# Kernel optimization log

Hardware: AMD Instinct MI355X
Metric: run time of the kernel (lower is better)

Reference implementation:

```python
import jax, jax.numpy as jnp
import numpy as np

B, T, D, H1, H2, O = 256, 200, 1250, 100, 20, 2
P = 0.2  # dropout prob (training=True in the original forward)


def setup_inputs() -> dict:
    key = jax.random.key(0)
    ks = jax.random.split(key, 13)
    s1 = 1.0 / np.sqrt(H1)  # torch nn.RNN init: U(-1/sqrt(hidden), 1/sqrt(hidden))
    s2 = 1.0 / np.sqrt(H2)
    sf = 1.0 / np.sqrt(H2)  # fc fan_in = 20
    u = lambda k, shape, s: jax.random.uniform(k, shape, jnp.float32, -s, s)
    keep = 1.0 - P
    return {
        "x": jax.random.normal(ks[0], (B, T, D), jnp.float32),
        "W_ih1": u(ks[1], (H1, D), s1),
        "W_hh1": u(ks[2], (H1, H1), s1),
        "b_ih1": u(ks[3], (H1,), s1),
        "b_hh1": u(ks[4], (H1,), s1),
        "W_ih2": u(ks[5], (H2, H1), s2),
        "W_hh2": u(ks[6], (H2, H2), s2),
        "b_ih2": u(ks[7], (H2,), s2),
        "b_hh2": u(ks[8], (H2,), s2),
        "W_fc": u(ks[9], (O, H2), sf),
        "b_fc": u(ks[10], (O,), sf),
        # pre-sampled inverted-dropout masks (training=True), scaled by 1/keep
        "mask1": jax.random.bernoulli(ks[11], keep, (B, T, H1)).astype(jnp.float32) / keep,
        "mask2": jax.random.bernoulli(ks[12], keep, (B, T, H2)).astype(jnp.float32) / keep,
    }


def _relu_rnn(x, W_ih, W_hh, b_ih, b_hh):
    # x: [B,T,Din] -> outputs [B,T,H]. Hoist the input projection out of the scan.
    pre = jnp.einsum("btd,hd->bth", x, W_ih) + b_ih + b_hh  # [B,T,H]
    h0 = jnp.zeros((x.shape[0], W_hh.shape[0]), x.dtype)

    def step(h, pre_t):
        h = jax.nn.relu(pre_t + h @ W_hh.T)
        return h, h

    _, out = jax.lax.scan(step, h0, jnp.swapaxes(pre, 0, 1))  # [T,B,H]
    return jnp.swapaxes(out, 0, 1)


def reference(x, W_ih1, W_hh1, b_ih1, b_hh1, W_ih2, W_hh2, b_ih2, b_hh2,
              W_fc, b_fc, mask1, mask2):
    out = _relu_rnn(x, W_ih1, W_hh1, b_ih1, b_hh1) * mask1          # rnn1 + dropout
    out = _relu_rnn(out, W_ih2, W_hh2, b_ih2, b_hh2) * mask2        # rnn2 + dropout
    return out[:, -1, :] @ W_fc.T + b_fc                            # fc on last step
```

## Files before the change

kernel.cpp:

```cpp
#include <hip/hip_runtime.h>

#define NB 256
#define TT 200
#define DD 1250
#define H1 100
#define H2 20
#define NO 2

#define BM 64
#define GRID_A (51200 / BM)
#define KC 64
#define NCH 20
#define WR 112
#define KPAD 1280

typedef __attribute__((ext_vector_type(4))) float f32x4;
typedef __attribute__((ext_vector_type(8))) short s16x8;

__device__ __forceinline__ unsigned short f2bf(float f) {
    unsigned u = __builtin_bit_cast(unsigned, f);
    u += 0x7FFFu + ((u >> 16) & 1u);
    return (unsigned short)(u >> 16);
}
__device__ __forceinline__ float bf2f(unsigned short s) {
    unsigned u = ((unsigned)s) << 16;
    return __builtin_bit_cast(float, u);
}

#define GLL(srcp, dstp) __builtin_amdgcn_global_load_lds( \
    (const __attribute__((address_space(1))) void*)(srcp), \
    (__attribute__((address_space(3))) void*)(dstp), 16, 0, 0)

#define STEP_BARRIER() do {                                             \
    asm volatile("s_waitcnt lgkmcnt(0)\n\ts_barrier" ::: "memory");     \
    __builtin_amdgcn_sched_barrier(0);                                  \
} while (0)

__global__ void prep_w(const float* __restrict__ Wih1, unsigned short* __restrict__ w_ws)
{
    const int idx = blockIdx.x * 256 + threadIdx.x;
    if (idx >= WR * KPAD / 4) return;
    const int r  = idx / (KPAD / 4);
    const int k4 = (idx - r * (KPAD / 4)) * 4;
    unsigned short o[4];
    #pragma unroll
    for (int e = 0; e < 4; ++e) {
        const int k = k4 + e;
        o[e] = (r < H1 && k < DD) ? f2bf(Wih1[r * DD + k]) : (unsigned short)0;
    }
    uint2 pk;
    pk.x = (unsigned)o[0] | ((unsigned)o[1] << 16);
    pk.y = (unsigned)o[2] | ((unsigned)o[3] << 16);
    *(uint2*)&w_ws[r * KPAD + k4] = pk;
}

__launch_bounds__(256, 4)
__global__ void gemm_pre(const float* __restrict__ x,
                         const unsigned short* __restrict__ w_ws,
                         unsigned short* __restrict__ preT)
{
    __shared__ __align__(16) float          a_sf[2][BM * 64];
    __shared__ __align__(16) unsigned short w_sh[2][WR * 64];

    const int tid = threadIdx.x;
    const int bid = blockIdx.x;
    const int wv  = tid >> 6;
    const int ln  = tid & 63;
    const int c16 = ln & 15;
    const int kgrp = ln >> 4;

    f32x4 acc[7];
    #pragma unroll
    for (int i = 0; i < 7; ++i)
        #pragma unroll
        for (int c = 0; c < 4; ++c) acc[i][c] = 0.f;

    auto agll = [&](int k0, int buf) {
        #pragma unroll
        for (int q = 0; q < 4; ++q) {
            const int idx  = tid + q * 256;
            const int row  = idx >> 4;
            const int segp = idx & 15;
            const int segl = segp ^ (row & 15);
            const float* src = x + (size_t)(bid * BM + row) * DD + k0 + segl * 4;
            GLL(src, &a_sf[buf][idx * 4]);
        }
    };
    auto wgll = [&](int k0, int buf) {
        #pragma unroll
        for (int q = 0; q < 4; ++q) {
            const int idx = tid + q * 256;
            if (idx < WR * 8) {
                const int row = idx >> 3;
                const int c8p = idx & 7;
                const int c8l = c8p ^ (row & 7);
                const unsigned short* src = w_ws + row * KPAD + k0 + c8l * 8;
                GLL(src, &w_sh[buf][idx * 8]);
            }
        }
    };

    auto mfma_chunk = [&](int buf) {
        #pragma unroll
        for (int s = 0; s < 2; ++s) {
            const int row_a = wv * 16 + c16;
            const int sb = s * 8 + kgrp * 2;
            const int sp0 = (sb + 0) ^ (row_a & 15);
            const int sp1 = (sb + 1) ^ (row_a & 15);
            const float4 av0 = *(const float4*)&a_sf[buf][row_a * 64 + sp0 * 4];
            const float4 av1 = *(const float4*)&a_sf[buf][row_a * 64 + sp1 * 4];
            const s16x8 af = {
                (short)f2bf(av0.x), (short)f2bf(av0.y),
                (short)f2bf(av0.z), (short)f2bf(av0.w),
                (short)f2bf(av1.x), (short)f2bf(av1.y),
                (short)f2bf(av1.z), (short)f2bf(av1.w) };
            #pragma unroll
            for (int nt = 0; nt < 7; ++nt) {
                const int row_b = nt * 16 + c16;
                const int c8  = s * 4 + kgrp;
                const int c8p = c8 ^ (row_b & 7);
                const s16x8 bf = *(const s16x8*)&w_sh[buf][row_b * 64 + c8p * 8];
                acc[nt] = __builtin_amdgcn_mfma_f32_16x16x32_bf16(af, bf, acc[nt], 0, 0, 0);
            }
        }
    };

    float4 ta[4];
    #pragma unroll
    for (int q = 0; q < 4; ++q) {
        const int idx  = tid + q * 256;
        const int row  = idx >> 4;
        const int segl = idx & 15;
        const int gk   = 19 * KC + segl * 4;
        const float* xp = x + (size_t)(bid * BM + row) * DD + gk;
        float4 v;
        v.x = (gk + 0 < DD) ? xp[0] : 0.f;
        v.y = (gk + 1 < DD) ? xp[1] : 0.f;
        v.z = (gk + 2 < DD) ? xp[2] : 0.f;
        v.w = (gk + 3 < DD) ? xp[3] : 0.f;
        ta[q] = v;
    }

    agll(0, 0);
    wgll(0, 0);

    for (int kc = 0; kc < 19; ++kc) {
        const int buf = kc & 1;
        __syncthreads();
        if (kc + 1 < 19) agll((kc + 1) * KC, buf ^ 1);
        wgll((kc + 1) * KC, buf ^ 1);
        mfma_chunk(buf);
    }

    #pragma unroll
    for (int q = 0; q < 4; ++q) {
        const int idx  = tid + q * 256;
        const int row  = idx >> 4;
        const int segl = idx & 15;
        const int sp   = segl ^ (row & 15);
        *(float4*)&a_sf[1][row * 64 + sp * 4] = ta[q];
    }
    __syncthreads();
    mfma_chunk(1);

    const int rg = bid * BM + wv * 16 + (kgrp << 2);
    #pragma unroll
    for (int nt = 0; nt < 7; ++nt) {
        const int col = nt * 16 + c16;
        if (col < H1) {
            #pragma unroll
            for (int r = 0; r < 4; ++r)
                preT[(size_t)(rg + r) * H1 + col] = f2bf(acc[nt][r]);
        }
    }
}

#define FMA4(W, PTR) { const float4 hv_ = *(const float4*)(PTR);            \
    a0 = fmaf((W).x, hv_.x, a0); a1 = fmaf((W).y, hv_.y, a1);               \
    a2 = fmaf((W).z, hv_.z, a2); a3 = fmaf((W).w, hv_.w, a3); }

#define CH 8
#define NCHK 25

__launch_bounds__(320, 1)
__global__ void scan_rnn(const unsigned short* __restrict__ preT,
                         const float* __restrict__ Whh1,
                         const float* __restrict__ bih1,
                         const float* __restrict__ bhh1,
                         const float* __restrict__ Wih2,
                         const float* __restrict__ Whh2,
                         const float* __restrict__ bih2,
                         const float* __restrict__ bhh2,
                         const float* __restrict__ Wfc,
                         const float* __restrict__ bfc,
                         const float* __restrict__ mask1,
                         const float* __restrict__ mask2,
                         float* __restrict__ out)
{
    __shared__ alignas(16) float h1_s[2][104];
    __shared__ alignas(16) float c_s[2][120];
    __shared__ alignas(16) float h2f_s[H2];
    __shared__ alignas(16) float m_lds[2][CH * H1];
    __shared__ alignas(16) float p_lds[2][CH * H1];

    const int tid = threadIdx.x;
    const int b   = blockIdx.x;
    const float* m1b = mask1 + (size_t)b * TT * H1;
    const unsigned short* pTb = preT + (size_t)b * TT * H1;

    const int h = tid >> 1;
    const int p = tid & 1;
    const bool l1t = (tid < 200);
    const bool l2t = (tid >= 256 && tid < 256 + 2 * H2);
    const int k2 = (tid - 256) >> 1;
    const int p3 = (tid - 256) & 1;

    float4 w00{}, w01{}, w02{}, w03{}, w04{}, w05{}, w06{}, w07{},
           w08{}, w09{}, w10{}, w11{}, w12{}, w13{}, w14{};
    float b1 = 0.f, b2 = 0.f;

    if (l1t) {
        const float* wr = Whh1 + h * H1 + p * 52;
        w00 = *(const float4*)(wr +  0); w01 = *(const float4*)(wr +  4);
        w02 = *(const float4*)(wr +  8); w03 = *(const float4*)(wr + 12);
        w04 = *(const float4*)(wr + 16); w05 = *(const float4*)(wr + 20);
        w06 = *(const float4*)(wr + 24); w07 = *(const float4*)(wr + 28);
        w08 = *(const float4*)(wr + 32); w09 = *(const float4*)(wr + 36);
        w10 = *(const float4*)(wr + 40); w11 = *(const float4*)(wr + 44);
        if (p == 0) { w12 = *(const float4*)(wr + 48); b1 = bih1[h] + bhh1[h]; }
    } else if (l2t) {
        if (p3 == 0) {
            const float* wr = Wih2 + k2 * H1;
            w00 = *(const float4*)(wr +  0); w01 = *(const float4*)(wr +  4);
            w02 = *(const float4*)(wr +  8); w03 = *(const float4*)(wr + 12);
            w04 = *(const float4*)(wr + 16); w05 = *(const float4*)(wr + 20);
            w06 = *(const float4*)(wr + 24); w07 = *(const float4*)(wr + 28);
            w08 = *(const float4*)(wr + 32); w09 = *(const float4*)(wr + 36);
            w10 = *(const float4*)(wr + 40); w11 = *(const float4*)(wr + 44);
            w12 = *(const float4*)(wr + 48); w13 = *(const float4*)(wr + 52);
            w14 = *(const float4*)(wr + 56);
            b2 = bih2[k2] + bhh2[k2];
        } else {
            const float* wr = Wih2 + k2 * H1 + 60;
            w00 = *(const float4*)(wr +  0); w01 = *(const float4*)(wr +  4);
            w02 = *(const float4*)(wr +  8); w03 = *(const float4*)(wr + 12);
            w04 = *(const float4*)(wr + 16); w05 = *(const float4*)(wr + 20);
            w06 = *(const float4*)(wr + 24); w07 = *(const float4*)(wr + 28);
            w08 = *(const float4*)(wr + 32); w09 = *(const float4*)(wr + 36);
            const float* wh = Whh2 + k2 * H2;
            w10 = *(const float4*)(wh +  0); w11 = *(const float4*)(wh +  4);
            w12 = *(const float4*)(wh +  8); w13 = *(const float4*)(wh + 12);
            w14 = *(const float4*)(wh + 16);
        }
    }

    for (int i = tid; i < 104; i += 320) { h1_s[0][i] = 0.f; h1_s[1][i] = 0.f; }
    for (int i = tid; i < 120; i += 320) { c_s[0][i] = 0.f; c_s[1][i] = 0.f; }

    if (tid < 200) {
        const float4 mv = *(const float4*)&m1b[tid * 4];
        *(float4*)&m_lds[0][tid * 4] = mv;
    } else if (tid < 300) {
        const s16x8 pv = *(const s16x8*)&pTb[(tid - 200) * 8];
        float* dst = &p_lds[0][(tid - 200) * 8];
        *(float4*)dst       = make_float4(bf2f(pv[0]), bf2f(pv[1]), bf2f(pv[2]), bf2f(pv[3]));
        *(float4*)(dst + 4) = make_float4(bf2f(pv[4]), bf2f(pv[5]), bf2f(pv[6]), bf2f(pv[7]));
    }
    __syncthreads();

    int buf = 0;
    for (int c = 0; c < NCHK; ++c) {
        const bool more = (c + 1 < NCHK);
        float4 mst{}; s16x8 pst{};

        #pragma unroll
        for (int u = 0; u < CH; ++u) {
            const int t = c * CH + u;
            const int cur = t & 1, nxt = cur ^ 1;

            if (u > 0) STEP_BARRIER();

            if (u == 0 && more) {
                const int base = (c + 1) * (CH * H1);
                if (tid < 200)      mst = *(const float4*)&m1b[base + tid * 4];
                else if (tid < 300) pst = *(const s16x8*)&pTb[base + (tid - 200) * 8];
            }

            if (l1t) {
                float a0 = (p == 0) ? (p_lds[buf][u * H1 + h] + b1) : 0.f;
                const float mv = (p == 1) ? m_lds[buf][u * H1 + h] : 0.f;
                float a1 = 0.f, a2 = 0.f, a3 = 0.f;
                const float* hb = &h1_s[cur][p * 52];
                FMA4(w00, hb +  0); FMA4(w01, hb +  4); FMA4(w02, hb +  8);
                FMA4(w03, hb + 12); FMA4(w04, hb + 16); FMA4(w05, hb + 20);
                FMA4(w06, hb + 24); FMA4(w07, hb + 28); FMA4(w08, hb + 32);
                FMA4(w09, hb + 36); FMA4(w10, hb + 40); FMA4(w11, hb + 44);
                FMA4(w12, hb + 48);
                float part = (a0 + a1) + (a2 + a3);
                float tot  = part + __shfl_xor(part, 1);
                tot = fmaxf(tot, 0.f);
                if (p == 0) h1_s[nxt][h] = tot;
                else        c_s[nxt][h] = tot * mv;
            }

            if (l2t && t >= 1) {
                float a0 = (p3 == 0) ? b2 : 0.f;
                float a1 = 0.f, a2 = 0.f, a3 = 0.f;
                const float* cb = &c_s[cur][p3 * 60];
                FMA4(w00, cb +  0); FMA4(w01, cb +  4); FMA4(w02, cb +  8);
                FMA4(w03, cb + 12); FMA4(w04, cb + 16); FMA4(w05, cb + 20);
                FMA4(w06, cb + 24); FMA4(w07, cb + 28); FMA4(w08, cb + 32);
                FMA4(w09, cb + 36); FMA4(w10, cb + 40); FMA4(w11, cb + 44);
                FMA4(w12, cb + 48); FMA4(w13, cb + 52); FMA4(w14, cb + 56);
                float part = (a0 + a1) + (a2 + a3);
                part += __shfl_xor(part, 1);
                const float h2v = fmaxf(part, 0.f);
                if (p3 == 0) c_s[nxt][100 + k2] = h2v;
            }
        }

        if (more) {
            if (tid < 200) {
                *(float4*)&m_lds[buf ^ 1][tid * 4] = mst;
            } else if (tid < 300) {
                float* dst = &p_lds[buf ^ 1][(tid - 200) * 8];
                *(float4*)dst       = make_float4(bf2f(pst[0]), bf2f(pst[1]), bf2f(pst[2]), bf2f(pst[3]));
                *(float4*)(dst + 4) = make_float4(bf2f(pst[4]), bf2f(pst[5]), bf2f(pst[6]), bf2f(pst[7]));
            }
            buf ^= 1;
        }
        __syncthreads();
    }

    {
        const int cur = TT & 1;
        if (l2t) {
            float a0 = (p3 == 0) ? b2 : 0.f;
            float a1 = 0.f, a2 = 0.f, a3 = 0.f;
            const float* cb = &c_s[cur][p3 * 60];
            FMA4(w00, cb +  0); FMA4(w01, cb +  4); FMA4(w02, cb +  8);
            FMA4(w03, cb + 12); FMA4(w04, cb + 16); FMA4(w05, cb + 20);
            FMA4(w06, cb + 24); FMA4(w07, cb + 28); FMA4(w08, cb + 32);
            FMA4(w09, cb + 36); FMA4(w10, cb + 40); FMA4(w11, cb + 44);
            FMA4(w12, cb + 48); FMA4(w13, cb + 52); FMA4(w14, cb + 56);
            float part = (a0 + a1) + (a2 + a3);
            part += __shfl_xor(part, 1);
            if (p3 == 0) h2f_s[k2] = fmaxf(part, 0.f);
        }
        __syncthreads();
    }

    if (tid < NO) {
        const float* m2 = mask2 + ((size_t)b * TT + (TT - 1)) * H2;
        float s = bfc[tid];
        #pragma unroll
        for (int k = 0; k < H2; ++k)
            s = fmaf(Wfc[tid * H2 + k], h2f_s[k] * m2[k], s);
        out[b * NO + tid] = s;
    }
}

extern "C" void kernel_launch(void* const* d_in, const int* in_sizes, int n_in,
                              void* d_out, int out_size, void* d_ws, size_t ws_size,
                              hipStream_t stream) {
    const float* x     = (const float*)d_in[0];
    const float* Wih1  = (const float*)d_in[1];
    const float* Whh1  = (const float*)d_in[2];
    const float* bih1  = (const float*)d_in[3];
    const float* bhh1  = (const float*)d_in[4];
    const float* Wih2  = (const float*)d_in[5];
    const float* Whh2  = (const float*)d_in[6];
    const float* bih2  = (const float*)d_in[7];
    const float* bhh2  = (const float*)d_in[8];
    const float* Wfc   = (const float*)d_in[9];
    const float* bfc   = (const float*)d_in[10];
    const float* mask1 = (const float*)d_in[11];
    const float* mask2 = (const float*)d_in[12];
    float* out = (float*)d_out;

    unsigned short* preT = (unsigned short*)d_ws;
    unsigned short* w_ws = (unsigned short*)((char*)d_ws + 10240000);

    prep_w  <<<dim3((WR * KPAD / 4 + 255) / 256), dim3(256), 0, stream>>>(Wih1, w_ws);
    gemm_pre<<<dim3(GRID_A), dim3(256), 0, stream>>>(x, w_ws, preT);
    scan_rnn<<<dim3(NB), dim3(320), 0, stream>>>(preT, Whh1, bih1, bhh1,
                                                 Wih2, Whh2, bih2, bhh2,
                                                 Wfc, bfc, mask1, mask2, out);
}
```

Measured before the change: 169.2 us.

## Batch 16 sequences per block and run recurrent matmuls on MFMA

The scan kernel now processes 16 batch rows per block instead of one. The per-step recurrent products for both RNN layers run as bf16 MFMA tiles, with the hidden state kept in bf16 in LDS, replacing per-thread fp32 FMA dot products. The layer-1 bias is folded into the GEMM epilogue, and pre-activation and mask chunks are staged with async global-to-LDS loads. The grid shrinks to 16 blocks, so most CUs sit idle during the scan, and bf16 hidden states add rounding error.

```diff
diff --git a/kernel.cpp b/kernel.cpp
--- a/kernel.cpp
+++ b/kernel.cpp
@@ -13,6 +13,12 @@
 #define NCH 20
 #define WR 112
 #define KPAD 1280
+#define PROWS 104
+
+#define G 16
+#define SCH 4
+#define SNCHK 50
+#define HS 136
 
 typedef __attribute__((ext_vector_type(4))) float f32x4;
 typedef __attribute__((ext_vector_type(8))) short s16x8;
@@ -57,6 +63,8 @@
 __launch_bounds__(256, 4)
 __global__ void gemm_pre(const float* __restrict__ x,
                          const unsigned short* __restrict__ w_ws,
+                         const float* __restrict__ bih1,
+                         const float* __restrict__ bhh1,
                          unsigned short* __restrict__ preT)
 {
     __shared__ __align__(16) float          a_sf[2][BM * 64];
@@ -74,6 +82,13 @@
     for (int i = 0; i < 7; ++i)
         #pragma unroll
         for (int c = 0; c < 4; ++c) acc[i][c] = 0.f;
+
+    float bias[7];
+    #pragma unroll
+    for (int nt = 0; nt < 7; ++nt) {
+        const int col = nt * 16 + c16;
+        bias[nt] = (col < H1) ? (bih1[col] + bhh1[col]) : 0.f;
+    }
 
     auto agll = [&](int k0, int buf) {
         #pragma unroll
@@ -170,23 +185,14 @@
         if (col < H1) {
             #pragma unroll
             for (int r = 0; r < 4; ++r)
-                preT[(size_t)(rg + r) * H1 + col] = f2bf(acc[nt][r]);
-        }
-    }
-}
-
-#define FMA4(W, PTR) { const float4 hv_ = *(const float4*)(PTR);            \
-    a0 = fmaf((W).x, hv_.x, a0); a1 = fmaf((W).y, hv_.y, a1);               \
-    a2 = fmaf((W).z, hv_.z, a2); a3 = fmaf((W).w, hv_.w, a3); }
-
-#define CH 8
-#define NCHK 25
-
-__launch_bounds__(320, 1)
+                preT[(size_t)(rg + r) * PROWS + col] = f2bf(acc[nt][r] + bias[nt]);
+        }
+    }
+}
+
+__launch_bounds__(256, 1)
 __global__ void scan_rnn(const unsigned short* __restrict__ preT,
                          const float* __restrict__ Whh1,
-                         const float* __restrict__ bih1,
-                         const float* __restrict__ bhh1,
                          const float* __restrict__ Wih2,
                          const float* __restrict__ Whh2,
                          const float* __restrict__ bih2,
@@ -197,166 +203,201 @@
                          const float* __restrict__ mask2,
                          float* __restrict__ out)
 {
-    __shared__ alignas(16) float h1_s[2][104];
-    __shared__ alignas(16) float c_s[2][120];
-    __shared__ alignas(16) float h2f_s[H2];
-    __shared__ alignas(16) float m_lds[2][CH * H1];
-    __shared__ alignas(16) float p_lds[2][CH * H1];
+    __shared__ __align__(16) unsigned short H1s[2][G * HS];
+    __shared__ __align__(16) unsigned short Cs [2][G * HS];
+    __shared__ __align__(16) unsigned short PREs[2][SCH * G * PROWS];
+    __shared__ __align__(16) float MASKs[2][SCH * G * H1];
 
     const int tid = threadIdx.x;
-    const int b   = blockIdx.x;
-    const float* m1b = mask1 + (size_t)b * TT * H1;
-    const unsigned short* pTb = preT + (size_t)b * TT * H1;
-
-    const int h = tid >> 1;
-    const int p = tid & 1;
-    const bool l1t = (tid < 200);
-    const bool l2t = (tid >= 256 && tid < 256 + 2 * H2);
-    const int k2 = (tid - 256) >> 1;
-    const int p3 = (tid - 256) & 1;
-
-    float4 w00{}, w01{}, w02{}, w03{}, w04{}, w05{}, w06{}, w07{},
-           w08{}, w09{}, w10{}, w11{}, w12{}, w13{}, w14{};
-    float b1 = 0.f, b2 = 0.f;
-
-    if (l1t) {
-        const float* wr = Whh1 + h * H1 + p * 52;
-        w00 = *(const float4*)(wr +  0); w01 = *(const float4*)(wr +  4);
-        w02 = *(const float4*)(wr +  8); w03 = *(const float4*)(wr + 12);
-        w04 = *(const float4*)(wr + 16); w05 = *(const float4*)(wr + 20);
-        w06 = *(const float4*)(wr + 24); w07 = *(const float4*)(wr + 28);
-        w08 = *(const float4*)(wr + 32); w09 = *(const float4*)(wr + 36);
-        w10 = *(const float4*)(wr + 40); w11 = *(const float4*)(wr + 44);
-        if (p == 0) { w12 = *(const float4*)(wr + 48); b1 = bih1[h] + bhh1[h]; }
-    } else if (l2t) {
-        if (p3 == 0) {
-            const float* wr = Wih2 + k2 * H1;
-            w00 = *(const float4*)(wr +  0); w01 = *(const float4*)(wr +  4);
-            w02 = *(const float4*)(wr +  8); w03 = *(const float4*)(wr + 12);
-            w04 = *(const float4*)(wr + 16); w05 = *(const float4*)(wr + 20);
-            w06 = *(const float4*)(wr + 24); w07 = *(const float4*)(wr + 28);
-            w08 = *(const float4*)(wr + 32); w09 = *(const float4*)(wr + 36);
-            w10 = *(const float4*)(wr + 40); w11 = *(const float4*)(wr + 44);
-            w12 = *(const float4*)(wr + 48); w13 = *(const float4*)(wr + 52);
-            w14 = *(const float4*)(wr + 56);
-            b2 = bih2[k2] + bhh2[k2];
-        } else {
-            const float* wr = Wih2 + k2 * H1 + 60;
-            w00 = *(const float4*)(wr +  0); w01 = *(const float4*)(wr +  4);
-            w02 = *(const float4*)(wr +  8); w03 = *(const float4*)(wr + 12);
-            w04 = *(const float4*)(wr + 16); w05 = *(const float4*)(wr + 20);
-            w06 = *(const float4*)(wr + 24); w07 = *(const float4*)(wr + 28);
-            w08 = *(const float4*)(wr + 32); w09 = *(const float4*)(wr + 36);
-            const float* wh = Whh2 + k2 * H2;
-            w10 = *(const float4*)(wh +  0); w11 = *(const float4*)(wh +  4);
-            w12 = *(const float4*)(wh +  8); w13 = *(const float4*)(wh + 12);
-            w14 = *(const float4*)(wh + 16);
-        }
-    }
-
-    for (int i = tid; i < 104; i += 320) { h1_s[0][i] = 0.f; h1_s[1][i] = 0.f; }
-    for (int i = tid; i < 120; i += 320) { c_s[0][i] = 0.f; c_s[1][i] = 0.f; }
-
-    if (tid < 200) {
-        const float4 mv = *(const float4*)&m1b[tid * 4];
-        *(float4*)&m_lds[0][tid * 4] = mv;
-    } else if (tid < 300) {
-        const s16x8 pv = *(const s16x8*)&pTb[(tid - 200) * 8];
-        float* dst = &p_lds[0][(tid - 200) * 8];
-        *(float4*)dst       = make_float4(bf2f(pv[0]), bf2f(pv[1]), bf2f(pv[2]), bf2f(pv[3]));
-        *(float4*)(dst + 4) = make_float4(bf2f(pv[4]), bf2f(pv[5]), bf2f(pv[6]), bf2f(pv[7]));
-    }
+    const int b0  = blockIdx.x * G;
+    const int wv  = tid >> 6;
+    const int ln  = tid & 63;
+    const int g   = ln & 15;
+    const int ro  = ln >> 4;
+
+    s16x8 a1f[2][4] = {};
+    #pragma unroll
+    for (int ti = 0; ti < 2; ++ti) {
+        const int rt = 2 * wv + ti;
+        if (rt < 7) {
+            const int row = rt * 16 + g;
+            #pragma unroll
+            for (int kt = 0; kt < 4; ++kt) {
+                const int kb = kt * 32 + ro * 8;
+                s16x8 f = {};
+                if (row < H1) {
+                    #pragma unroll
+                    for (int j = 0; j < 8; ++j) {
+                        const int k = kb + j;
+                        const float v = (k < H1) ? Whh1[row * H1 + k] : 0.f;
+                        f[j] = (short)f2bf(v);
+                    }
+                }
+                a1f[ti][kt] = f;
+            }
+        }
+    }
+    s16x8 a2f[2][4] = {};
+    f32x4 b2v[2] = {};
+    if (wv == 3) {
+        #pragma unroll
+        for (int ti = 0; ti < 2; ++ti) {
+            const int row = ti * 16 + g;
+            #pragma unroll
+            for (int kt = 0; kt < 4; ++kt) {
+                const int kb = kt * 32 + ro * 8;
+                s16x8 f = {};
+                if (row < H2) {
+                    #pragma unroll
+                    for (int j = 0; j < 8; ++j) {
+                        const int k = kb + j;
+                        float v = 0.f;
+                        if (k < H1) v = Wih2[row * H1 + k];
+                        else if (k < H1 + H2) v = Whh2[row * H2 + (k - H1)];
+                        f[j] = (short)f2bf(v);
+                    }
+                }
+                a2f[ti][kt] = f;
+            }
+            const int rb2 = ti * 16 + ro * 4;
+            #pragma unroll
+            for (int r = 0; r < 4; ++r)
+                b2v[ti][r] = (rb2 + r < H2) ? (bih2[rb2 + r] + bhh2[rb2 + r]) : 0.f;
+        }
+    }
+
+    for (int i = tid; i < G * HS; i += 256) {
+        H1s[0][i] = 0; H1s[1][i] = 0; Cs[0][i] = 0; Cs[1][i] = 0;
+    }
+
+    auto stage = [&](int c, int pb) {
+        for (int s = tid; s < SCH * G * 13; s += 256) {
+            const int ug = s / 13, ss = s - ug * 13;
+            const int u = ug >> 4, gg = ug & 15;
+            const unsigned short* src = preT +
+                ((size_t)(b0 + gg) * TT + (c * SCH + u)) * PROWS + ss * 8;
+            GLL(src, &PREs[pb][s * 8]);
+        }
+        for (int s = tid; s < SCH * G * 25; s += 256) {
+            const int ug = s / 25, ss = s - ug * 25;
+            const int u = ug >> 4, gg = ug & 15;
+            const float* src = mask1 +
+                ((size_t)(b0 + gg) * TT + (c * SCH + u)) * H1 + ss * 4;
+            GLL(src, &MASKs[pb][s * 4]);
+        }
+    };
+
+    stage(0, 0);
     __syncthreads();
 
-    int buf = 0;
-    for (int c = 0; c < NCHK; ++c) {
-        const bool more = (c + 1 < NCHK);
-        float4 mst{}; s16x8 pst{};
-
-        #pragma unroll
-        for (int u = 0; u < CH; ++u) {
-            const int t = c * CH + u;
+    for (int c = 0; c < SNCHK; ++c) {
+        const int pb = c & 1;
+        #pragma unroll
+        for (int u = 0; u < SCH; ++u) {
+            const int t = c * SCH + u;
             const int cur = t & 1, nxt = cur ^ 1;
-
             if (u > 0) STEP_BARRIER();
-
-            if (u == 0 && more) {
-                const int base = (c + 1) * (CH * H1);
-                if (tid < 200)      mst = *(const float4*)&m1b[base + tid * 4];
-                else if (tid < 300) pst = *(const s16x8*)&pTb[base + (tid - 200) * 8];
-            }
-
-            if (l1t) {
-                float a0 = (p == 0) ? (p_lds[buf][u * H1 + h] + b1) : 0.f;
-                const float mv = (p == 1) ? m_lds[buf][u * H1 + h] : 0.f;
-                float a1 = 0.f, a2 = 0.f, a3 = 0.f;
-                const float* hb = &h1_s[cur][p * 52];
-                FMA4(w00, hb +  0); FMA4(w01, hb +  4); FMA4(w02, hb +  8);
-                FMA4(w03, hb + 12); FMA4(w04, hb + 16); FMA4(w05, hb + 20);
-                FMA4(w06, hb + 24); FMA4(w07, hb + 28); FMA4(w08, hb + 32);
-                FMA4(w09, hb + 36); FMA4(w10, hb + 40); FMA4(w11, hb + 44);
-                FMA4(w12, hb + 48);
-                float part = (a0 + a1) + (a2 + a3);
-                float tot  = part + __shfl_xor(part, 1);
-                tot = fmaxf(tot, 0.f);
-                if (p == 0) h1_s[nxt][h] = tot;
-                else        c_s[nxt][h] = tot * mv;
-            }
-
-            if (l2t && t >= 1) {
-                float a0 = (p3 == 0) ? b2 : 0.f;
-                float a1 = 0.f, a2 = 0.f, a3 = 0.f;
-                const float* cb = &c_s[cur][p3 * 60];
-                FMA4(w00, cb +  0); FMA4(w01, cb +  4); FMA4(w02, cb +  8);
-                FMA4(w03, cb + 12); FMA4(w04, cb + 16); FMA4(w05, cb + 20);
-                FMA4(w06, cb + 24); FMA4(w07, cb + 28); FMA4(w08, cb + 32);
-                FMA4(w09, cb + 36); FMA4(w10, cb + 40); FMA4(w11, cb + 44);
-                FMA4(w12, cb + 48); FMA4(w13, cb + 52); FMA4(w14, cb + 56);
-                float part = (a0 + a1) + (a2 + a3);
-                part += __shfl_xor(part, 1);
-                const float h2v = fmaxf(part, 0.f);
-                if (p3 == 0) c_s[nxt][100 + k2] = h2v;
-            }
-        }
-
-        if (more) {
-            if (tid < 200) {
-                *(float4*)&m_lds[buf ^ 1][tid * 4] = mst;
-            } else if (tid < 300) {
-                float* dst = &p_lds[buf ^ 1][(tid - 200) * 8];
-                *(float4*)dst       = make_float4(bf2f(pst[0]), bf2f(pst[1]), bf2f(pst[2]), bf2f(pst[3]));
-                *(float4*)(dst + 4) = make_float4(bf2f(pst[4]), bf2f(pst[5]), bf2f(pst[6]), bf2f(pst[7]));
-            }
-            buf ^= 1;
+            if (u == 0 && c + 1 < SNCHK) stage(c + 1, pb ^ 1);
+
+            s16x8 bfr[4];
+            #pragma unroll
+            for (int kt = 0; kt < 4; ++kt)
+                bfr[kt] = *(const s16x8*)&H1s[cur][g * HS + kt * 32 + ro * 8];
+
+            #pragma unroll
+            for (int ti = 0; ti < 2; ++ti) {
+                const int rt = 2 * wv + ti;
+                if (rt < 7) {
+                    f32x4 acc = {0.f, 0.f, 0.f, 0.f};
+                    #pragma unroll
+                    for (int kt = 0; kt < 4; ++kt)
+                        acc = __builtin_amdgcn_mfma_f32_16x16x32_bf16(
+                            a1f[ti][kt], bfr[kt], acc, 0, 0, 0);
+                    const int rb = rt * 16 + ro * 4;
+                    const uint2 pr = *(const uint2*)&PREs[pb][(u * 16 + g) * PROWS + rb];
+                    const float4 mk = *(const float4*)&MASKs[pb][(u * 16 + g) * H1 + rb];
+                    const float v0 = fmaxf(acc[0] + bf2f((unsigned short)(pr.x)), 0.f);
+                    const float v1 = fmaxf(acc[1] + bf2f((unsigned short)(pr.x >> 16)), 0.f);
+                    const float v2 = fmaxf(acc[2] + bf2f((unsigned short)(pr.y)), 0.f);
+                    const float v3 = fmaxf(acc[3] + bf2f((unsigned short)(pr.y >> 16)), 0.f);
+                    if (rb < H1) {
+                        uint2 hw, ow;
+                        hw.x = (unsigned)f2bf(v0) | ((unsigned)f2bf(v1) << 16);
+                        hw.y = (unsigned)f2bf(v2) | ((unsigned)f2bf(v3) << 16);
+                        ow.x = (unsigned)f2bf(v0 * mk.x) | ((unsigned)f2bf(v1 * mk.y) << 16);
+                        ow.y = (unsigned)f2bf(v2 * mk.z) | ((unsigned)f2bf(v3 * mk.w) << 16);
+                        *(uint2*)&H1s[nxt][g * HS + rb] = hw;
+                        *(uint2*)&Cs[nxt][g * HS + rb] = ow;
+                    }
+                }
+            }
+
+            if (wv == 3 && t >= 1) {
+                s16x8 cfr[4];
+                #pragma unroll
+                for (int kt = 0; kt < 4; ++kt)
+                    cfr[kt] = *(const s16x8*)&Cs[cur][g * HS + kt * 32 + ro * 8];
+                #pragma unroll
+                for (int ti = 0; ti < 2; ++ti) {
+                    f32x4 acc = {0.f, 0.f, 0.f, 0.f};
+                    #pragma unroll
+                    for (int kt = 0; kt < 4; ++kt)
+                        acc = __builtin_amdgcn_mfma_f32_16x16x32_bf16(
+                            a2f[ti][kt], cfr[kt], acc, 0, 0, 0);
+                    const int rb = ti * 16 + ro * 4;
+                    if (rb < H2) {
+                        const float v0 = fmaxf(acc[0] + b2v[ti][0], 0.f);
+                        const float v1 = fmaxf(acc[1] + b2v[ti][1], 0.f);
+                        const float v2 = fmaxf(acc[2] + b2v[ti][2], 0.f);
+                        const float v3 = fmaxf(acc[3] + b2v[ti][3], 0.f);
+                        uint2 w2;
+                        w2.x = (unsigned)f2bf(v0) | ((unsigned)f2bf(v1) << 16);
+                        w2.y = (unsigned)f2bf(v2) | ((unsigned)f2bf(v3) << 16);
+                        *(uint2*)&Cs[nxt][g * HS + H1 + rb] = w2;
+                    }
+                }
+            }
         }
         __syncthreads();
     }
 
-    {
-        const int cur = TT & 1;
-        if (l2t) {
-            float a0 = (p3 == 0) ? b2 : 0.f;
-            float a1 = 0.f, a2 = 0.f, a3 = 0.f;
-            const float* cb = &c_s[cur][p3 * 60];
-            FMA4(w00, cb +  0); FMA4(w01, cb +  4); FMA4(w02, cb +  8);
-            FMA4(w03, cb + 12); FMA4(w04, cb + 16); FMA4(w05, cb + 20);
-            FMA4(w06, cb + 24); FMA4(w07, cb + 28); FMA4(w08, cb + 32);
-            FMA4(w09, cb + 36); FMA4(w10, cb + 40); FMA4(w11, cb + 44);
-            FMA4(w12, cb + 48); FMA4(w13, cb + 52); FMA4(w14, cb + 56);
-            float part = (a0 + a1) + (a2 + a3);
-            part += __shfl_xor(part, 1);
-            if (p3 == 0) h2f_s[k2] = fmaxf(part, 0.f);
-        }
-        __syncthreads();
-    }
-
-    if (tid < NO) {
-        const float* m2 = mask2 + ((size_t)b * TT + (TT - 1)) * H2;
-        float s = bfc[tid];
-        #pragma unroll
-        for (int k = 0; k < H2; ++k)
-            s = fmaf(Wfc[tid * H2 + k], h2f_s[k] * m2[k], s);
-        out[b * NO + tid] = s;
+    if (wv == 3) {
+        s16x8 cfr[4];
+        #pragma unroll
+        for (int kt = 0; kt < 4; ++kt)
+            cfr[kt] = *(const s16x8*)&Cs[0][g * HS + kt * 32 + ro * 8];
+        #pragma unroll
+        for (int ti = 0; ti < 2; ++ti) {
+            f32x4 acc = {0.f, 0.f, 0.f, 0.f};
+            #pragma unroll
+            for (int kt = 0; kt < 4; ++kt)
+                acc = __builtin_amdgcn_mfma_f32_16x16x32_bf16(
+                    a2f[ti][kt], cfr[kt], acc, 0, 0, 0);
+            const int rb = ti * 16 + ro * 4;
+            if (rb < H2) {
+                const float v0 = fmaxf(acc[0] + b2v[ti][0], 0.f);
+                const float v1 = fmaxf(acc[1] + b2v[ti][1], 0.f);
+                const float v2 = fmaxf(acc[2] + b2v[ti][2], 0.f);
+                const float v3 = fmaxf(acc[3] + b2v[ti][3], 0.f);
+                uint2 w2;
+                w2.x = (unsigned)f2bf(v0) | ((unsigned)f2bf(v1) << 16);
+                w2.y = (unsigned)f2bf(v2) | ((unsigned)f2bf(v3) << 16);
+                *(uint2*)&Cs[1][g * HS + H1 + rb] = w2;
+            }
+        }
+    }
+    __syncthreads();
+
+    if (tid < G * NO) {
+        const int bb = tid >> 1, o = tid & 1;
+        float s = bfc[o];
+        #pragma unroll
+        for (int k = 0; k < H2; ++k) {
+            const float h2k = bf2f(Cs[1][bb * HS + H1 + k]);
+            const float m2k = mask2[((size_t)(b0 + bb) * TT + (TT - 1)) * H2 + k];
+            s = fmaf(Wfc[o * H2 + k], h2k * m2k, s);
+        }
+        out[(b0 + bb) * NO + o] = s;
     }
 }
 
@@ -379,11 +420,11 @@
     float* out = (float*)d_out;
 
     unsigned short* preT = (unsigned short*)d_ws;
-    unsigned short* w_ws = (unsigned short*)((char*)d_ws + 10240000);
+    unsigned short* w_ws = (unsigned short*)((char*)d_ws + 10649600);
 
     prep_w  <<<dim3((WR * KPAD / 4 + 255) / 256), dim3(256), 0, stream>>>(Wih1, w_ws);
-    gemm_pre<<<dim3(GRID_A), dim3(256), 0, stream>>>(x, w_ws, preT);
-    scan_rnn<<<dim3(NB), dim3(320), 0, stream>>>(preT, Whh1, bih1, bhh1,
-                                                 Wih2, Whh2, bih2, bhh2,
-                                                 Wfc, bfc, mask1, mask2, out);
-}
+    gemm_pre<<<dim3(GRID_A), dim3(256), 0, stream>>>(x, w_ws, bih1, bhh1, preT);
+    scan_rnn<<<dim3(NB / G), dim3(256), 0, stream>>>(preT, Whh1, Wih2, Whh2,
+                                                     bih2, bhh2, Wfc, bfc,
+                                                     mask1, mask2, out);
+}
```

Measured after the change: 224.9 us. 32.9% more time.
